# Kernel optimization log

Measured on AMD Instinct MI355X. Metric: run time of the kernel, lower is better.

## Reference

```python
import jax, jax.numpy as jnp
import numpy as np

EMBED_DIM = 1024
NUM_HEADS = 16
HEAD_DIM = EMBED_DIM // NUM_HEADS
B, S = 4, 2048


def setup_inputs() -> dict:
    key = jax.random.key(0)
    ks = jax.random.split(key, 11)
    d = EMBED_DIM
    s = 1.0 / np.sqrt(d)
    return {
        "query": jax.random.normal(ks[0], (B, S, d), jnp.float32),
        "key": jax.random.normal(ks[1], (B, S, d), jnp.float32),
        "value": jax.random.normal(ks[2], (B, S, d), jnp.float32),
        "Wq": jax.random.normal(ks[3], (d, d), jnp.float32) * s,
        "bq": jnp.zeros((d,), jnp.float32),
        "Wk": jax.random.normal(ks[4], (d, d), jnp.float32) * s,
        "bk": jnp.zeros((d,), jnp.float32),
        "Wv": jax.random.normal(ks[5], (d, d), jnp.float32) * s,
        "bv": jnp.zeros((d,), jnp.float32),
        "Wo": jax.random.normal(ks[6], (d, d), jnp.float32) * s,
        "bo": jnp.zeros((d,), jnp.float32),
    }


def reference(query, key, value, Wq, bq, Wk, bk, Wv, bv, Wo, bo):
    b, t, d = query.shape
    s = key.shape[1]
    h, hd = NUM_HEADS, HEAD_DIM
    # Linear projections (torch Linear: x @ W.T + b)
    q = (query @ Wq.T + bq).reshape(b, t, h, hd).transpose(0, 2, 1, 3)  # [B,H,T,hd]
    k = (key @ Wk.T + bk).reshape(b, s, h, hd).transpose(0, 2, 1, 3)    # [B,H,S,hd]
    v = (value @ Wv.T + bv).reshape(b, s, h, hd).transpose(0, 2, 1, 3)  # [B,H,S,hd]
    scale = 1.0 / np.sqrt(hd).astype(np.float32)
    attn = jnp.einsum('bhtd,bhsd->bhts', q, k) * scale  # [B,H,T,S]
    attn = jax.nn.softmax(attn, axis=-1)
    out = jnp.einsum('bhts,bhsd->bhtd', attn, v)        # [B,H,T,hd]
    out = out.transpose(0, 2, 1, 3).reshape(b, t, d)    # [B,T,D]
    out = out @ Wo.T + bo
    return out
```

## Files before the change

### kernel.cpp

```cpp
#include <hip/hip_runtime.h>
#include <hip/hip_bf16.h>
#include <stdint.h>

typedef __attribute__((ext_vector_type(8))) short short8;
typedef __attribute__((ext_vector_type(4))) float floatx4;
typedef __attribute__((ext_vector_type(16))) float floatx16;
typedef __attribute__((ext_vector_type(4))) uint16_t ushort4v;

#define MFMA16(a, b, c) __builtin_amdgcn_mfma_f32_16x16x32_bf16((a), (b), (c), 0, 0, 0)
#define MFMA32(a, b, c) __builtin_amdgcn_mfma_f32_32x32x16_bf16((a), (b), (c), 0, 0, 0)

#define GLOAD_LDS16(g, l)                                                          \
  __builtin_amdgcn_global_load_lds(                                                \
      (const __attribute__((address_space(1))) uint32_t*)(g),                      \
      (__attribute__((address_space(3))) uint32_t*)(l), 16, 0, 0)

#define CVTPK(lo_, hi_, out_) \
  asm("v_cvt_pk_bf16_f32 %0, %1, %2" : "=v"(out_) : "v"(lo_), "v"(hi_))
#define SWAP32(a_, b_) \
  asm("v_permlane32_swap_b32 %0, %1" : "+v"(a_), "+v"(b_))

__device__ __forceinline__ uint16_t f2bf(float x) {
  union { float f; uint32_t u; } c; c.f = x;
  return (uint16_t)((c.u + 0x7FFFu + ((c.u >> 16) & 1u)) >> 16);
}

__global__ void cvt3_k(const float* __restrict__ s0, const float* __restrict__ s1,
                       const float* __restrict__ s2, uint16_t* __restrict__ dst, int n4) {
  const float* src = blockIdx.z == 0 ? s0 : (blockIdx.z == 1 ? s1 : s2);
  uint16_t* d = dst + (size_t)blockIdx.z * 8388608;
  int stride = gridDim.x * blockDim.x;
  for (int i = blockIdx.x * blockDim.x + threadIdx.x; i < n4; i += stride) {
    float4 v = ((const float4*)src)[i];
    ushort4v o;
    o.x = f2bf(v.x); o.y = f2bf(v.y); o.z = f2bf(v.z); o.w = f2bf(v.w);
    ((ushort4v*)d)[i] = o;
  }
}
__global__ void cvt4_k(const float* __restrict__ s0, const float* __restrict__ s1,
                       const float* __restrict__ s2, const float* __restrict__ s3,
                       uint16_t* __restrict__ dst, int n4) {
  const float* src = blockIdx.z == 0 ? s0 : (blockIdx.z == 1 ? s1 : (blockIdx.z == 2 ? s2 : s3));
  uint16_t* d = dst + (size_t)blockIdx.z * 1048576;
  int stride = gridDim.x * blockDim.x;
  for (int i = blockIdx.x * blockDim.x + threadIdx.x; i < n4; i += stride) {
    float4 v = ((const float4*)src)[i];
    ushort4v o;
    o.x = f2bf(v.x); o.y = f2bf(v.y); o.z = f2bf(v.z); o.w = f2bf(v.w);
    ((ushort4v*)d)[i] = o;
  }
}

template <int OUT_BF16>
__device__ __forceinline__ void gemm_body(const uint16_t* __restrict__ A,
                                          const uint16_t* __restrict__ W,
                                          const float* __restrict__ bias,
                                          void* __restrict__ Cout, float scale) {
  constexpr int N = 1024, K = 1024;
  __shared__ uint16_t As[128 * 32];
  __shared__ uint16_t Bs[128 * 32];
  const int t = threadIdx.x;
  const int l = t & 63;
  const int w = t >> 6;
  const int wr = w >> 1, wc = w & 1;
  const int l16 = l & 15, lhi = l >> 4;
  const int brow = blockIdx.y * 128;
  const int bcol = blockIdx.x * 128;

  floatx4 acc[4][4] = {};

  for (int k0 = 0; k0 < K; k0 += 32) {
#pragma unroll
    for (int j = 0; j < 2; ++j) {
      int c = j * 256 + t;
      int row = c >> 2;
      int ko = (c & 3) * 8;
      const uint16_t* ga = A + (size_t)(brow + row) * K + k0 + ko;
      const uint16_t* gb = W + (size_t)(bcol + row) * K + k0 + ko;
      uint16_t* la = As + (size_t)(j * 256 + w * 64) * 8;
      uint16_t* lb = Bs + (size_t)(j * 256 + w * 64) * 8;
      GLOAD_LDS16(ga, la);
      GLOAD_LDS16(gb, lb);
    }
    __syncthreads();

    short8 a[4], b[4];
#pragma unroll
    for (int m = 0; m < 4; ++m)
      a[m] = *(const short8*)&As[(wr * 64 + m * 16 + l16) * 32 + lhi * 8];
#pragma unroll
    for (int n = 0; n < 4; ++n)
      b[n] = *(const short8*)&Bs[(wc * 64 + n * 16 + l16) * 32 + lhi * 8];
#pragma unroll
    for (int m = 0; m < 4; ++m)
#pragma unroll
      for (int n = 0; n < 4; ++n)
        acc[m][n] = MFMA16(a[m], b[n], acc[m][n]);
    __syncthreads();
  }

#pragma unroll
  for (int n = 0; n < 4; ++n) {
    int col = bcol + wc * 64 + n * 16 + l16;
    float bv = bias[col];
#pragma unroll
    for (int m = 0; m < 4; ++m) {
#pragma unroll
      for (int j = 0; j < 4; ++j) {
        int row = brow + wr * 64 + m * 16 + lhi * 4 + j;
        float v = (acc[m][n][j] + bv) * scale;
        if (OUT_BF16)
          ((uint16_t*)Cout)[(size_t)row * N + col] = f2bf(v);
        else
          ((float*)Cout)[(size_t)row * N + col] = v;
      }
    }
  }
}

__global__ __launch_bounds__(256)
void gemm_qkv_k(const uint16_t* __restrict__ XQ, const uint16_t* __restrict__ XK,
                const uint16_t* __restrict__ XV, const uint16_t* __restrict__ WQ,
                const uint16_t* __restrict__ WK, const uint16_t* __restrict__ WV,
                const float* __restrict__ bq, const float* __restrict__ bk,
                const float* __restrict__ bv, uint16_t* __restrict__ QP,
                uint16_t* __restrict__ KP, uint16_t* __restrict__ VP, float qscale) {
  const uint16_t *A, *W; const float* bi; uint16_t* C; float sc;
  if (blockIdx.z == 0)      { A = XQ; W = WQ; bi = bq; C = QP; sc = qscale; }
  else if (blockIdx.z == 1) { A = XK; W = WK; bi = bk; C = KP; sc = 1.0f; }
  else                      { A = XV; W = WV; bi = bv; C = VP; sc = 1.0f; }
  gemm_body<1>(A, W, bi, C, sc);
}

__global__ __launch_bounds__(256)
void gemm_o_k(const uint16_t* __restrict__ A, const uint16_t* __restrict__ W,
              const float* __restrict__ bias, float* __restrict__ Cout) {
  gemm_body<0>(A, W, bias, Cout, 1.0f);
}

__global__ __launch_bounds__(256)
void vtrans_k(const uint16_t* __restrict__ VP, uint16_t* __restrict__ VT) {
  __shared__ uint16_t T[64][66];
  const int t = threadIdx.x;
  const int bh = blockIdx.y;
  const int s0 = blockIdx.x * 64;
  const int b = bh >> 4, h = bh & 15;
  const size_t src = ((size_t)b * 2048 + s0) * 1024 + (size_t)h * 64;
#pragma unroll
  for (int it = 0; it < 2; ++it) {
    int u = it * 256 + t;
    int s = u >> 3;
    int d0 = (u & 7) * 8;
    short8 v = *(const short8*)(VP + src + (size_t)s * 1024 + d0);
#pragma unroll
    for (int i = 0; i < 8; ++i) T[s][d0 + i] = (uint16_t)v[i];
  }
  __syncthreads();
  const size_t dst = (size_t)bh * 131072 + s0;
#pragma unroll
  for (int it = 0; it < 2; ++it) {
    int u = it * 256 + t;
    int d = u >> 3;
    int ss = (u & 7) * 8;
    union { uint16_t u16[8]; short8 s8; } pk;
#pragma unroll
    for (int i = 0; i < 8; ++i) pk.u16[i] = T[ss + i][d];
    *(short8*)(VT + dst + (size_t)d * 2048 + ss) = pk.s8;
  }
}

__global__ __launch_bounds__(256)
void attn_k(const uint16_t* __restrict__ Qp, const uint16_t* __restrict__ Kp,
            const uint16_t* __restrict__ Vt, uint16_t* __restrict__ AO) {
  __shared__ uint16_t Kl[2][64 * 64];
  __shared__ uint16_t Vl[2][64 * 64];

  const int t = threadIdx.x;
  const int l = t & 63, w = t >> 6;
  const int l32 = l & 31, hi = l >> 5;

  const int f = blockIdx.y * 16 + blockIdx.x;
  const int virt = (f & 7) * 128 + (f >> 3);
  const int vx = virt & 15;
  const int vy = virt >> 4;

  const int q0 = vx * 128 + w * 32;
  const size_t base = (size_t)(vy >> 4) * 2048 * 1024 + (size_t)(vy & 15) * 64;
  const size_t vbg = (size_t)vy * 131072;

  union PAu { uint32_t u[4]; short8 s; };

  const int cA = t, cB = 256 + t;
  const uint16_t* pK0 = Kp + base + (size_t)(cA >> 3) * 1024 + ((cA ^ (cA >> 3)) & 7) * 8;
  const uint16_t* pK1 = Kp + base + (size_t)(cB >> 3) * 1024 + ((cB ^ (cB >> 3)) & 7) * 8;
  const uint16_t* pV0 = Vt + vbg + (size_t)(cA >> 3) * 2048 + ((cA ^ (cA >> 3)) & 7) * 8;
  const uint16_t* pV1 = Vt + vbg + (size_t)(cB >> 3) * 2048 + ((cB ^ (cB >> 3)) & 7) * 8;

#define STAGE_ALL(NB)                                                \
  {                                                                  \
    GLOAD_LDS16(pK0, &Kl[NB][(size_t)(0 * 256 + w * 64) * 8]);       \
    GLOAD_LDS16(pK1, &Kl[NB][(size_t)(1 * 256 + w * 64) * 8]);       \
    GLOAD_LDS16(pV0, &Vl[NB][(size_t)(0 * 256 + w * 64) * 8]);       \
    GLOAD_LDS16(pV1, &Vl[NB][(size_t)(1 * 256 + w * 64) * 8]);       \
    pK0 += 65536; pK1 += 65536;               \
    pV0 += 64; pV1 += 64;                   \
  }

  short8 qf[4];
#pragma unroll
  for (int ks = 0; ks < 4; ++ks)
    qf[ks] = *(const short8*)(Qp + base + (size_t)(q0 + l32) * 1024 + ks * 16 + hi * 8);

  floatx16 of0 = {}, of1 = {};
  floatx16 osum = {};

  short8 ones;
#pragma unroll
  for (int i = 0; i < 8; ++i) ones[i] = (short)0x3F80;

  STAGE_ALL(0);
  __syncthreads();

#define STEP(CUR, PF)                                                                 \
  {                                                                                   \
    if (PF) STAGE_ALL(CUR ^ 1);                                                       \
    floatx16 sf0 = {}, sf1 = {};                                                      \
    __builtin_amdgcn_s_setprio(1);                                                    \
    _Pragma("unroll") for (int ks = 0; ks < 4; ++ks) {                                \
      int kb = (ks * 16 + hi * 8) * 2;                                                \
      int swz = (l32 & 7) << 4;                                                       \
      short8 kf0 = *(const short8*)((char*)Kl[CUR] + ((l32 * 128 + kb) ^ swz));       \
      short8 kf1 = *(const short8*)((char*)Kl[CUR] + (((32 + l32) * 128 + kb) ^ swz));\
      sf0 = MFMA32(kf0, qf[ks], sf0);                                                 \
      sf1 = MFMA32(kf1, qf[ks], sf1);                                                 \
    }                                                                                 \
    __builtin_amdgcn_s_setprio(0);                                                    \
    _Pragma("unroll") for (int r = 0; r < 16; ++r) {                                  \
      sf0[r] = __builtin_amdgcn_exp2f(sf0[r]);                                        \
      sf1[r] = __builtin_amdgcn_exp2f(sf1[r]);                                        \
    }                                                                                 \
    PAu pa[4];                                                                        \
    _Pragma("unroll") for (int sb = 0; sb < 2; ++sb) {                                \
      const floatx16& sv = sb ? sf1 : sf0;                                            \
      _Pragma("unroll") for (int ks = 0; ks < 2; ++ks) {                              \
        uint32_t a0, a1, b0, b1;                                                      \
        CVTPK(sv[8 * ks + 0], sv[8 * ks + 1], a0);                                    \
        CVTPK(sv[8 * ks + 2], sv[8 * ks + 3], a1);                                    \
        CVTPK(sv[8 * ks + 4], sv[8 * ks + 5], b0);                                    \
        CVTPK(sv[8 * ks + 6], sv[8 * ks + 7], b1);                                    \
        SWAP32(a0, b0);                                                               \
        SWAP32(a1, b1);                                                               \
        pa[sb * 2 + ks].u[0] = a0; pa[sb * 2 + ks].u[1] = a1;                         \
        pa[sb * 2 + ks].u[2] = b0; pa[sb * 2 + ks].u[3] = b1;                         \
      }                                                                               \
    }                                                                                 \
    __builtin_amdgcn_s_setprio(1);                                                    \
    _Pragma("unroll") for (int kk = 0; kk < 4; ++kk) {                                \
      osum = MFMA32(pa[kk].s, ones, osum);                                            \
      int sbyte = (kk * 16 + hi * 8) * 2;                                             \
      int swz = (l32 & 7) << 4;                                                       \
      short8 vf0 = *(const short8*)((char*)Vl[CUR] + ((l32 * 128 + sbyte) ^ swz));    \
      short8 vf1 = *(const short8*)((char*)Vl[CUR] + (((32 + l32) * 128 + sbyte) ^ swz)); \
      of0 = MFMA32(pa[kk].s, vf0, of0);                                               \
      of1 = MFMA32(pa[kk].s, vf1, of1);                                               \
    }                                                                                 \
    __builtin_amdgcn_s_setprio(0);                                                    \
    __syncthreads();                                                                  \
  }

  for (int it = 0; it < 16; ++it) {
    STEP(0, 1);
    STEP(1, it < 15);
  }

#pragma unroll
  for (int r = 0; r < 16; ++r) {
    float rinv = 1.0f / osum[r];
    int qrow = q0 + (r & 3) + 8 * (r >> 2) + 4 * hi;
    AO[base + (size_t)qrow * 1024 + l32]      = f2bf(of0[r] * rinv);
    AO[base + (size_t)qrow * 1024 + 32 + l32] = f2bf(of1[r] * rinv);
  }
#undef STAGE_ALL
#undef STEP
}

extern "C" void kernel_launch(void* const* d_in, const int* in_sizes, int n_in,
                              void* d_out, int out_size, void* d_ws, size_t ws_size,
                              hipStream_t stream) {
  const float* q  = (const float*)d_in[0];
  const float* k  = (const float*)d_in[1];
  const float* v  = (const float*)d_in[2];
  const float* Wq = (const float*)d_in[3];
  const float* bq = (const float*)d_in[4];
  const float* Wk = (const float*)d_in[5];
  const float* bk = (const float*)d_in[6];
  const float* Wv = (const float*)d_in[7];
  const float* bv = (const float*)d_in[8];
  const float* Wo = (const float*)d_in[9];
  const float* bo = (const float*)d_in[10];

  const size_t MB = 1ull << 20;
  char* ws = (char*)d_ws;
  uint16_t* XQ  = (uint16_t*)(ws + 0 * MB);
  uint16_t* XK  = (uint16_t*)(ws + 16 * MB);
  uint16_t* XV  = (uint16_t*)(ws + 32 * MB);
  uint16_t* WQb = (uint16_t*)(ws + 48 * MB);
  uint16_t* WKb = (uint16_t*)(ws + 50 * MB);
  uint16_t* WVb = (uint16_t*)(ws + 52 * MB);
  uint16_t* WOb = (uint16_t*)(ws + 54 * MB);
  uint16_t* QP  = (uint16_t*)(ws + 56 * MB);
  uint16_t* KP  = (uint16_t*)(ws + 72 * MB);
  uint16_t* VP  = (uint16_t*)(ws + 88 * MB);
  uint16_t* AO  = XQ;
  uint16_t* VT  = XK;

  const int NTOK = 4 * 2048;
  const int D = 1024;
  const int nBig = NTOK * D / 4;
  const int nW = D * D / 4;
  const float qscale = 0.125f * 1.4426950408889634f;

  cvt3_k<<<dim3(2048, 1, 3), dim3(256), 0, stream>>>(q, k, v, XQ, nBig);
  cvt4_k<<<dim3(1024, 1, 4), dim3(256), 0, stream>>>(Wq, Wk, Wv, Wo, WQb, nW);

  gemm_qkv_k<<<dim3(D / 128, NTOK / 128, 3), dim3(256), 0, stream>>>(
      XQ, XK, XV, WQb, WKb, WVb, bq, bk, bv, QP, KP, VP, qscale);

  vtrans_k<<<dim3(32, 64), dim3(256), 0, stream>>>(VP, VT);

  attn_k<<<dim3(16, 64), dim3(256), 0, stream>>>(QP, KP, VT, AO);

  gemm_o_k<<<dim3(D / 128, NTOK / 128), dim3(256), 0, stream>>>(AO, WOb, bo, (float*)d_out);
}
```

Baseline: 229.3 us.

## Double KV tile to 128 keys per stage with new LDS swizzle

The attention kernel now stages 128 keys of K and V per pipeline stage instead of 64. Each stage is processed as two 64-key halves between barriers, which halves the number of __syncthreads and stage-issue points. The LDS layout and swizzle are reworked to 256-byte rows with a 16-way XOR. Shared memory use doubles to 64KB per block, which may reduce occupancy.

```diff
diff --git a/kernel.cpp b/kernel.cpp
--- a/kernel.cpp
+++ b/kernel.cpp
@@ -172,8 +172,8 @@
 __global__ __launch_bounds__(256)
 void attn_k(const uint16_t* __restrict__ Qp, const uint16_t* __restrict__ Kp,
             const uint16_t* __restrict__ Vt, uint16_t* __restrict__ AO) {
-  __shared__ uint16_t Kl[2][64 * 64];
-  __shared__ uint16_t Vl[2][64 * 64];
+  __shared__ uint16_t Kl[2][64 * 128];
+  __shared__ uint16_t Vl[2][64 * 128];
 
   const int t = threadIdx.x;
   const int l = t & 63, w = t >> 6;
@@ -190,20 +190,25 @@
 
   union PAu { uint32_t u[4]; short8 s; };
 
-  const int cA = t, cB = 256 + t;
-  const uint16_t* pK0 = Kp + base + (size_t)(cA >> 3) * 1024 + ((cA ^ (cA >> 3)) & 7) * 8;
-  const uint16_t* pK1 = Kp + base + (size_t)(cB >> 3) * 1024 + ((cB ^ (cB >> 3)) & 7) * 8;
-  const uint16_t* pV0 = Vt + vbg + (size_t)(cA >> 3) * 2048 + ((cA ^ (cA >> 3)) & 7) * 8;
-  const uint16_t* pV1 = Vt + vbg + (size_t)(cB >> 3) * 2048 + ((cB ^ (cB >> 3)) & 7) * 8;
-
-#define STAGE_ALL(NB)                                                \
-  {                                                                  \
-    GLOAD_LDS16(pK0, &Kl[NB][(size_t)(0 * 256 + w * 64) * 8]);       \
-    GLOAD_LDS16(pK1, &Kl[NB][(size_t)(1 * 256 + w * 64) * 8]);       \
-    GLOAD_LDS16(pV0, &Vl[NB][(size_t)(0 * 256 + w * 64) * 8]);       \
-    GLOAD_LDS16(pV1, &Vl[NB][(size_t)(1 * 256 + w * 64) * 8]);       \
-    pK0 += 65536; pK1 += 65536;               \
-    pV0 += 64; pV1 += 64;                   \
+  const uint16_t* pK[4];
+  const uint16_t* pV[4];
+#pragma unroll
+  for (int i = 0; i < 4; ++i) {
+    int c = i * 256 + t;
+    int r = c >> 4, qs = c & 15;
+    int q0c = qs ^ (r & 15);
+    pK[i] = Kp + base + (size_t)(64 * (q0c >> 3) + r) * 1024 + (q0c & 7) * 8;
+    pV[i] = Vt + vbg + (size_t)r * 2048 + q0c * 8;
+  }
+
+#define STAGE_ALL(NB)                                                 \
+  {                                                                   \
+    _Pragma("unroll") for (int i = 0; i < 4; ++i) {                   \
+      GLOAD_LDS16(pK[i], &Kl[NB][(size_t)(i * 256 + w * 64) * 8]);    \
+      GLOAD_LDS16(pV[i], &Vl[NB][(size_t)(i * 256 + w * 64) * 8]);    \
+      pK[i] += 131072;                          \
+      pV[i] += 128;                              \
+    }                                                                 \
   }
 
   short8 qf[4];
@@ -218,19 +223,20 @@
 #pragma unroll
   for (int i = 0; i < 8; ++i) ones[i] = (short)0x3F80;
 
+  const int swzb = (l32 & 15);
+  const int krow = l32 * 256;
+
   STAGE_ALL(0);
   __syncthreads();
 
-#define STEP(CUR, PF)                                                                 \
+#define HALF(CUR, H)                                                                  \
   {                                                                                   \
-    if (PF) STAGE_ALL(CUR ^ 1);                                                       \
     floatx16 sf0 = {}, sf1 = {};                                                      \
     __builtin_amdgcn_s_setprio(1);                                                    \
     _Pragma("unroll") for (int ks = 0; ks < 4; ++ks) {                                \
-      int kb = (ks * 16 + hi * 8) * 2;                                                \
-      int swz = (l32 & 7) << 4;                                                       \
-      short8 kf0 = *(const short8*)((char*)Kl[CUR] + ((l32 * 128 + kb) ^ swz));       \
-      short8 kf1 = *(const short8*)((char*)Kl[CUR] + (((32 + l32) * 128 + kb) ^ swz));\
+      int kbyte = krow + (((H * 8 + 2 * ks + hi) ^ swzb) << 4);                       \
+      short8 kf0 = *(const short8*)((char*)Kl[CUR] + kbyte);                          \
+      short8 kf1 = *(const short8*)((char*)Kl[CUR] + kbyte + 8192);                   \
       sf0 = MFMA32(kf0, qf[ks], sf0);                                                 \
       sf1 = MFMA32(kf1, qf[ks], sf1);                                                 \
     }                                                                                 \
@@ -257,20 +263,26 @@
     __builtin_amdgcn_s_setprio(1);                                                    \
     _Pragma("unroll") for (int kk = 0; kk < 4; ++kk) {                                \
       osum = MFMA32(pa[kk].s, ones, osum);                                            \
-      int sbyte = (kk * 16 + hi * 8) * 2;                                             \
-      int swz = (l32 & 7) << 4;                                                       \
-      short8 vf0 = *(const short8*)((char*)Vl[CUR] + ((l32 * 128 + sbyte) ^ swz));    \
-      short8 vf1 = *(const short8*)((char*)Vl[CUR] + (((32 + l32) * 128 + sbyte) ^ swz)); \
+      int vbyte = krow + (((H * 8 + 2 * kk + hi) ^ swzb) << 4);                       \
+      short8 vf0 = *(const short8*)((char*)Vl[CUR] + vbyte);                          \
+      short8 vf1 = *(const short8*)((char*)Vl[CUR] + vbyte + 8192);                   \
       of0 = MFMA32(pa[kk].s, vf0, of0);                                               \
       of1 = MFMA32(pa[kk].s, vf1, of1);                                               \
     }                                                                                 \
     __builtin_amdgcn_s_setprio(0);                                                    \
+  }
+
+#define STEP128(CUR, PF)                                                              \
+  {                                                                                   \
+    if (PF) STAGE_ALL(CUR ^ 1);                                                       \
+    HALF(CUR, 0);                                                                     \
+    HALF(CUR, 1);                                                                     \
     __syncthreads();                                                                  \
   }
 
-  for (int it = 0; it < 16; ++it) {
-    STEP(0, 1);
-    STEP(1, it < 15);
+  for (int it = 0; it < 8; ++it) {
+    STEP128(0, 1);
+    STEP128(1, it < 7);
   }
 
 #pragma unroll
@@ -281,7 +293,8 @@
     AO[base + (size_t)qrow * 1024 + 32 + l32] = f2bf(of1[r] * rinv);
   }
 #undef STAGE_ALL
-#undef STEP
+#undef HALF
+#undef STEP128
 }
 
 extern "C" void kernel_launch(void* const* d_in, const int* in_sizes, int n_in,
```

Result: no change. 226.8 us (-1.1%).
